# Optimization experiments

Measured on AMD Instinct MI355X. Metric: run time of the kernel, lower is better.

The kernel has to match this reference:

```python
import jax, jax.numpy as jnp
import numpy as np
import math

B, H, N, D = 2, 16, 8192, 64
NUM_PROJS = 7
BLOCK = 256   # key block size
SAMPLE = 256  # number of sampled columns


def _gray_perm(n):
    # AngularLSH._unit_hamming_distance_array: Gray-code ordering of 2**n buckets
    a = np.array([0, 1], dtype=np.int32)
    for i in range(1, n):
        a = np.concatenate([a, a[::-1] + 2 ** i])
    return a

PERM = jnp.asarray(_gray_perm(NUM_PROJS))
ENC = jnp.asarray(2 ** np.arange(NUM_PROJS), dtype=jnp.int32)


def lsh_hash(x, proj_dir):
    # sign-bit angular LSH, then Gray-code remap so nearby buckets share bits
    bits = (jnp.einsum('bhnd,dr->bhnr', x, proj_dir) > 0).astype(jnp.int32)
    bin_ids = (bits * ENC).sum(-1)
    return PERM[bin_ids]


def take_seq(x, idx):
    # gather along the sequence axis (axis=2); idx is [B,H,M]
    return jnp.take_along_axis(x, idx[..., None], axis=2)


def setup_inputs() -> dict:
    key = jax.random.key(0)
    ks = jax.random.split(key, 5)
    return {
        'query': jax.random.normal(ks[0], (B, H, N, D), jnp.float32),
        'key': jax.random.normal(ks[1], (B, H, N, D), jnp.float32),
        'value': jax.random.normal(ks[2], (B, H, N, D), jnp.float32),
        'proj_dir': jax.random.normal(ks[3], (D + 1, NUM_PROJS), jnp.float32),
        'sampled_set': jax.random.randint(ks[4], (B, H, SAMPLE), 0, N),
    }


def reference(query, key, value, proj_dir, sampled_set):
    scale = D ** -0.5

    # asymmetric MIPS transform: key gets sqrt(max||k||^2 - ||k||^2), query gets 0
    k_norm = jnp.linalg.norm(key, axis=-1)                 # [B,H,N]
    k_max = jnp.max(k_norm, axis=-1, keepdims=True)        # [B,H,1]
    k_extra = jnp.sqrt(jnp.maximum(k_max ** 2 - k_norm ** 2, 0.0))
    key_aug = jnp.concatenate([key, k_extra[..., None]], axis=-1)
    query_aug = jnp.concatenate([query, jnp.zeros_like(query[..., :1])], axis=-1)

    # stable sort by LSH bucket; inverse permutation to un-sort queries at the end
    q_idx = jnp.argsort(lsh_hash(query_aug, proj_dir), axis=2, stable=True)
    k_idx = jnp.argsort(lsh_hash(key_aug, proj_dir), axis=2, stable=True)
    q_idx_inv = jnp.argsort(q_idx, axis=2, stable=True)

    q_s = take_seq(query, q_idx)
    k_s = take_seq(key, k_idx)
    v_s = take_seq(value, k_idx)

    nb = N // BLOCK      # number of key blocks (N divisible by BLOCK here)
    qbs = N // nb        # query block size

    # 1) block-diagonal exact attention over LSH-sorted blocks
    qb = q_s.reshape(B, H, nb, qbs, D)
    kb = k_s.reshape(B, H, nb, BLOCK, D)
    vb = v_s.reshape(B, H, nb, BLOCK, D)
    s_blk = jnp.einsum('bhgqd,bhgkd->bhgqk', qb, kb) * scale
    lse_blk = jax.nn.logsumexp(s_blk, axis=-1)             # [B,H,nb,qbs]
    attn_blk = jnp.einsum('bhgqk,bhgkd->bhgqd', jax.nn.softmax(s_blk, axis=-1), vb)
    attn_blk = attn_blk.reshape(B, H, N, D)
    lse_blk = lse_blk.reshape(B, H, N, 1)

    # 2) residual via uniformly sampled columns; mask out columns already in the
    #    query's own diagonal block to avoid double counting
    k_sub = take_seq(k_s, sampled_set)                     # [B,H,S,D]
    v_sub = take_seq(v_s, sampled_set)
    q_blk_id = jnp.arange(N) // qbs                        # [N]
    covered = q_blk_id[None, None, :, None] == (sampled_set // BLOCK)[:, :, None, :]
    bias = jnp.where(covered, jnp.finfo(q_s.dtype).min, 0.0)
    s_res = jnp.einsum('bhnd,bhsd->bhns', q_s, k_sub) * scale + bias
    # importance weight n_key/sample_size applied in log-space (approximate_unsampled)
    lse_res = jax.nn.logsumexp(s_res, axis=-1, keepdims=True) + math.log(N / SAMPLE)
    attn_res = jnp.einsum('bhns,bhsd->bhnd', jax.nn.softmax(s_res, axis=-1), v_sub)

    # add_self_attentions: merge the two softmax estimates in log-space
    c = 1.0 / (1.0 + jnp.exp(lse_res - lse_blk))
    attn = c * attn_blk + (1.0 - c) * attn_res

    # un-sort rows back to the original query order
    attn = take_seq(attn, q_idx_inv)
    return attn
```

## Files before the change

kernel.cpp:

```cpp
#include <hip/hip_runtime.h>
#include <hip/hip_bf16.h>
#include <math.h>

#define BD 2
#define HD 16
#define NSEQ 8192
#define DDIM 64
#define NPROJ 7
#define KBLK 256
#define NSAMP 256
#define NBH (BD*HD)
#define NB (NSEQ/KBLK)

typedef short bf16x8 __attribute__((ext_vector_type(8)));
typedef float f32x4 __attribute__((ext_vector_type(4)));

__device__ __forceinline__ unsigned int pk2bf(float a, float b) {
    union { __hip_bfloat162 h; unsigned int u; } t;
    t.h = __float22bfloat162_rn(make_float2(a, b));
    return t.u;
}

__global__ __launch_bounds__(256) void prelude_kernel(const float* __restrict__ q,
                                                      const float* __restrict__ k,
                                                      const float* __restrict__ pd,
                                                      float* __restrict__ kdots,
                                                      unsigned int* __restrict__ kmax_bits,
                                                      unsigned char* __restrict__ qh) {
    __shared__ float pds[(DDIM+1)*NPROJ];
    __shared__ float red[256];
    const int tid = threadIdx.x;
    for (int i = tid; i < (DDIM+1)*NPROJ; i += 256) pds[i] = pd[i];
    __syncthreads();

    const int lin = blockIdx.x * 256 + tid;
    const int bh = lin >> 13;

    float acc[NPROJ];
    float4 xv[16];

    {
        const float4* xp = (const float4*)(q + (size_t)lin * DDIM);
        #pragma unroll
        for (int j = 0; j < 16; ++j) xv[j] = xp[j];
        #pragma unroll
        for (int r = 0; r < NPROJ; ++r) acc[r] = 0.f;
        #pragma unroll
        for (int j = 0; j < 16; ++j) {
            float xs[4] = {xv[j].x, xv[j].y, xv[j].z, xv[j].w};
            #pragma unroll
            for (int c = 0; c < 4; ++c) {
                const int d = j*4 + c;
                #pragma unroll
                for (int r = 0; r < NPROJ; ++r) acc[r] += xs[c] * pds[d*NPROJ + r];
            }
        }
        int bin = 0;
        #pragma unroll
        for (int r = 0; r < NPROJ; ++r) bin |= (acc[r] > 0.f) << r;
        qh[lin] = (unsigned char)(bin ^ (bin >> 1));
    }

    float nr;
    {
        const float4* xp = (const float4*)(k + (size_t)lin * DDIM);
        #pragma unroll
        for (int j = 0; j < 16; ++j) xv[j] = xp[j];
        #pragma unroll
        for (int r = 0; r < NPROJ; ++r) acc[r] = 0.f;
        #pragma unroll
        for (int j = 0; j < 16; ++j) {
            float xs[4] = {xv[j].x, xv[j].y, xv[j].z, xv[j].w};
            #pragma unroll
            for (int c = 0; c < 4; ++c) {
                const int d = j*4 + c;
                #pragma unroll
                for (int r = 0; r < NPROJ; ++r) acc[r] += xs[c] * pds[d*NPROJ + r];
            }
        }
        float ss = 0.f;
        #pragma unroll
        for (int j = 0; j < 16; ++j) {
            float4 t = xv[j];
            ss += t.x*t.x + t.y*t.y + t.z*t.z + t.w*t.w;
        }
        nr = sqrtf(ss);
        float4* kd = (float4*)(kdots + (size_t)lin * 8);
        kd[0] = make_float4(acc[0], acc[1], acc[2], acc[3]);
        kd[1] = make_float4(acc[4], acc[5], acc[6], nr);
    }

    red[tid] = nr;
    __syncthreads();
    for (int s = 128; s > 0; s >>= 1) {
        if (tid < s) red[tid] = fmaxf(red[tid], red[tid+s]);
        __syncthreads();
    }
    if (tid == 0) atomicMax(&kmax_bits[bh], __float_as_uint(red[0]));
}

__global__ __launch_bounds__(256) void khash_kernel(const float* __restrict__ pd,
                                                    const float* __restrict__ kdots,
                                                    const unsigned int* __restrict__ kmax_bits,
                                                    unsigned char* __restrict__ kh) {
    const int lin = blockIdx.x * 256 + threadIdx.x;
    const int bh = lin >> 13;
    const float4* kd = (const float4*)(kdots + (size_t)lin * 8);
    float4 d0 = kd[0], d1 = kd[1];
    float acc[NPROJ] = {d0.x, d0.y, d0.z, d0.w, d1.x, d1.y, d1.z};
    const float kn = d1.w;
    const float km = __uint_as_float(kmax_bits[bh]);
    const float ex = sqrtf(fmaxf(km*km - kn*kn, 0.f));
    int bin = 0;
    #pragma unroll
    for (int r = 0; r < NPROJ; ++r) {
        acc[r] += ex * pd[DDIM*NPROJ + r];
        bin |= (acc[r] > 0.f) << r;
    }
    kh[lin] = (unsigned char)(bin ^ (bin >> 1));
}

__global__ __launch_bounds__(256) void sort_kernel(const unsigned char* __restrict__ qhash,
                                                   const unsigned char* __restrict__ khash,
                                                   int* __restrict__ qidx,
                                                   int* __restrict__ kidx) {
    __shared__ unsigned char hsh[NSEQ];
    __shared__ unsigned short cnt[128][264];
    __shared__ int base[128];
    __shared__ int wtot[2];
    const int bh = blockIdx.x, tid = threadIdx.x;
    const unsigned char* hash = blockIdx.y ? khash : qhash;
    int* idx = blockIdx.y ? kidx : qidx;

    {
        const uint4* src = (const uint4*)(hash + (size_t)bh * NSEQ);
        uint4* hdst = (uint4*)hsh;
        hdst[tid] = src[tid];
        hdst[tid + 256] = src[tid + 256];
        unsigned int* cz = (unsigned int*)&cnt[0][0];
        for (int i = tid; i < 128*264/2; i += 256) cz[i] = 0;
    }
    __syncthreads();
    {
        const unsigned char* s = hsh + tid*32;
        for (int i = 0; i < 32; ++i) cnt[s[i]][tid]++;
    }
    __syncthreads();

    int sc = 0, vv = 0;
    if (tid < 128) {
        unsigned run = 0;
        uint4* rp = (uint4*)cnt[tid];
        for (int wd = 0; wd < 32; ++wd) {
            uint4 x = rp[wd];
            unsigned v0 = x.x & 0xffffu, v1 = x.x >> 16;
            unsigned v2 = x.y & 0xffffu, v3 = x.y >> 16;
            unsigned v4 = x.z & 0xffffu, v5 = x.z >> 16;
            unsigned v6 = x.w & 0xffffu, v7 = x.w >> 16;
            unsigned p0 = run, p1 = p0+v0, p2 = p1+v1, p3 = p2+v2,
                     p4 = p3+v3, p5 = p4+v4, p6 = p5+v5, p7 = p6+v6;
            run = p7 + v7;
            x.x = p0 | (p1<<16); x.y = p2 | (p3<<16);
            x.z = p4 | (p5<<16); x.w = p6 | (p7<<16);
            rp[wd] = x;
        }
        vv = (int)run;
        sc = vv;
        #pragma unroll
        for (int d = 1; d < 64; d <<= 1) {
            int t = __shfl_up(sc, d, 64);
            if ((tid & 63) >= d) sc += t;
        }
        if ((tid & 63) == 63) wtot[tid >> 6] = sc;
    }
    __syncthreads();
    if (tid < 128) base[tid] = (sc - vv) + (tid >= 64 ? wtot[0] : 0);
    __syncthreads();
    {
        int* dst = idx + (size_t)bh * NSEQ;
        const unsigned char* s = hsh + tid*32;
        for (int i = 0; i < 32; ++i) {
            int h = s[i];
            int c = cnt[h][tid];
            cnt[h][tid] = (unsigned short)(c + 1);
            dst[base[h] + c] = tid*32 + i;
        }
    }
}

#define VSWZ(d) ((((d) >> 1) & 7) << 4)

__global__ __launch_bounds__(256) void respack_kernel(const float* __restrict__ k,
                                                      const float* __restrict__ v,
                                                      const int* __restrict__ samp,
                                                      const int* __restrict__ kidx,
                                                      char* __restrict__ kres,
                                                      char* __restrict__ vres) {
    const int bh = blockIdx.x, ch = blockIdx.y, tid = threadIdx.x;
    const size_t basef = (size_t)bh * NSEQ * DDIM;
    char* kimg = kres + (size_t)(bh*4 + ch) * 8192;
    char* vimg = vres + (size_t)(bh*4 + ch) * 8192;

    {
        const int kk = tid & 63, dc = tid >> 6;
        const int sp = samp[bh*NSAMP + ch*64 + kk];
        const int row = kidx[bh*NSEQ + sp];
        const float* kr = k + basef + (size_t)row*DDIM + dc*16;
        float4 f0 = ((const float4*)kr)[0], f1 = ((const float4*)kr)[1];
        float4 f2 = ((const float4*)kr)[2], f3 = ((const float4*)kr)[3];
        union { bf16x8 v8; unsigned int u[4]; } h0, h1;
        h0.u[0] = pk2bf(f0.x,f0.y); h0.u[1] = pk2bf(f0.z,f0.w);
        h0.u[2] = pk2bf(f1.x,f1.y); h0.u[3] = pk2bf(f1.z,f1.w);
        h1.u[0] = pk2bf(f2.x,f2.y); h1.u[1] = pk2bf(f2.z,f2.w);
        h1.u[2] = pk2bf(f3.x,f3.y); h1.u[3] = pk2bf(f3.z,f3.w);
        const int rb = kk*128 + dc*32, sw = (kk & 7) << 4;
        *(bf16x8*)(kimg + ((rb) ^ sw)) = h0.v8;
        *(bf16x8*)(kimg + ((rb + 16) ^ sw)) = h1.v8;
    }
    {
        const int vg = tid & 15, kq = tid >> 4;
        const int r0 = kidx[bh*NSEQ + samp[bh*NSAMP + ch*64 + kq*4 + 0]];
        const int r1 = kidx[bh*NSEQ + samp[bh*NSAMP + ch*64 + kq*4 + 1]];
        const int r2 = kidx[bh*NSEQ + samp[bh*NSAMP + ch*64 + kq*4 + 2]];
        const int r3 = kidx[bh*NSEQ + samp[bh*NSAMP + ch*64 + kq*4 + 3]];
        float4 x0 = *(const float4*)(v + basef + (size_t)r0*DDIM + vg*4);
        float4 x1 = *(const float4*)(v + basef + (size_t)r1*DDIM + vg*4);
        float4 x2 = *(const float4*)(v + basef + (size_t)r2*DDIM + vg*4);
        float4 x3 = *(const float4*)(v + basef + (size_t)r3*DDIM + vg*4);
        const float c0[4] = {x0.x, x0.y, x0.z, x0.w};
        const float c1[4] = {x1.x, x1.y, x1.z, x1.w};
        const float c2[4] = {x2.x, x2.y, x2.z, x2.w};
        const float c3[4] = {x3.x, x3.y, x3.z, x3.w};
        #pragma unroll
        for (int j = 0; j < 4; ++j) {
            const int d = vg*4 + j;
            unsigned h01 = pk2bf(c0[j], c1[j]);
            unsigned h23 = pk2bf(c2[j], c3[j]);
            *(uint2*)(vimg + ((d*128 + kq*8) ^ VSWZ(d))) = make_uint2(h01, h23);
        }
    }
}


#define PPITCH 80
#define LN32 3.46573590279972f

template<int PHASE>
__device__ __forceinline__ void chunk_compute(
    int lane, char* Pw, int ch,
    const bf16x8 (&qhf)[4][2], const bf16x8 (&qlf)[4][2],
    f32x4 (&O)[4][4], float (&lacc)[4],
    const float* maskF, const char* KhL, const char* VthL) {

    const int lr4 = lane >> 4;
    const int lc  = lane & 15;

    #pragma unroll
    for (int half = 0; half < 2; ++half) {
        #pragma unroll
        for (int m2 = 0; m2 < 2; ++m2) {
            const int mt = half*2 + m2;
            const int key = mt*16 + lc;
            const int ksw = (key & 7) << 4;
            bf16x8 ka0 = *(const bf16x8*)(KhL + ((key*128 +  0 + lr4*16) ^ ksw));
            bf16x8 ka1 = *(const bf16x8*)(KhL + ((key*128 + 64 + lr4*16) ^ ksw));
            float4 mk;
            if (PHASE) mk = *(const float4*)(maskF + ch*64 + mt*16 + lr4*4);
            #pragma unroll
            for (int qt = 0; qt < 4; ++qt) {
                f32x4 c = {0.f, 0.f, 0.f, 0.f};
                c = __builtin_amdgcn_mfma_f32_16x16x32_bf16(ka0, qhf[qt][0], c, 0, 0, 0);
                c = __builtin_amdgcn_mfma_f32_16x16x32_bf16(ka0, qlf[qt][0], c, 0, 0, 0);
                c = __builtin_amdgcn_mfma_f32_16x16x32_bf16(ka1, qhf[qt][1], c, 0, 0, 0);
                c = __builtin_amdgcn_mfma_f32_16x16x32_bf16(ka1, qlf[qt][1], c, 0, 0, 0);
                float e0, e1, e2, e3;
                if (PHASE) {
                    e0 = __expf(c[0] + LN32) * mk.x;
                    e1 = __expf(c[1] + LN32) * mk.y;
                    e2 = __expf(c[2] + LN32) * mk.z;
                    e3 = __expf(c[3] + LN32) * mk.w;
                } else {
                    e0 = __expf(c[0]); e1 = __expf(c[1]);
                    e2 = __expf(c[2]); e3 = __expf(c[3]);
                }
                lacc[qt] += (e0+e1) + (e2+e3);
                uint2 wv;
                wv.x = pk2bf(e0, e1);
                wv.y = pk2bf(e2, e3);
                const int qq = qt*16 + lc;
                *(uint2*)(Pw + qq*PPITCH + m2*32 + lr4*8) = wv;
            }
        }

        bf16x8 pf[4];
        #pragma unroll
        for (int qt = 0; qt < 4; ++qt)
            pf[qt] = *(const bf16x8*)(Pw + (qt*16 + lc)*PPITCH + lr4*16);

        __builtin_amdgcn_s_setprio(1);
        #pragma unroll
        for (int dt = 0; dt < 4; ++dt) {
            const int d = dt*16 + lc;
            const int a = (d*128 + half*64 + lr4*16) ^ VSWZ(d);
            bf16x8 vh = *(const bf16x8*)(VthL + a);
            #pragma unroll
            for (int qt = 0; qt < 4; ++qt) {
                O[qt][dt] = __builtin_amdgcn_mfma_f32_16x16x32_bf16(pf[qt], vh, O[qt][dt], 0, 0, 0);
            }
        }
        __builtin_amdgcn_s_setprio(0);
    }
}

__global__ __launch_bounds__(256, 2) void attn_kernel(const float* __restrict__ q,
                                                      const float* __restrict__ k,
                                                      const float* __restrict__ v,
                                                      const int* __restrict__ samp,
                                                      const int* __restrict__ qidx,
                                                      const int* __restrict__ kidx,
                                                      const char* __restrict__ kres,
                                                      const char* __restrict__ vres,
                                                      float* __restrict__ out) {
    __shared__ __align__(16) char KhL[8192];
    __shared__ __align__(16) char VthL[8192];
    __shared__ __align__(16) char PL[4][PPITCH*64];
    __shared__ int qidxL[256];
    __shared__ int kidxL[256];
    __shared__ float maskF[256];

    const int g = blockIdx.x, bh = blockIdx.y;
    const int tid = threadIdx.x;
    const int lane = tid & 63, w = tid >> 6;
    const int lr4 = lane >> 4, lc = lane & 15;
    const size_t basef = (size_t)bh * NSEQ * DDIM;

    qidxL[tid] = qidx[bh*NSEQ + g*KBLK + tid];
    kidxL[tid] = kidx[bh*NSEQ + g*KBLK + tid];
    {
        int sp = samp[bh*NSAMP + tid];
        maskF[tid] = ((sp >> 8) == g) ? 0.f : 1.f;
    }
    __syncthreads();

    bf16x8 qhf[4][2], qlf[4][2];
    #pragma unroll
    for (int qt = 0; qt < 4; ++qt) {
        const int qrow = qidxL[w*64 + qt*16 + lc];
        const float* qp = q + basef + (size_t)qrow*DDIM;
        #pragma unroll
        for (int ks = 0; ks < 2; ++ks) {
            const float* p = qp + ks*32 + lr4*8;
            float4 a = *(const float4*)p;
            float4 b = *(const float4*)(p + 4);
            float xs[8] = {a.x,a.y,a.z,a.w,b.x,b.y,b.z,b.w};
            union { bf16x8 v8; unsigned int u[4]; } hv, lv;
            #pragma unroll
            for (int j = 0; j < 4; ++j) {
                float s0 = xs[2*j]   * 0.125f;
                float s1 = xs[2*j+1] * 0.125f;
                unsigned hp = pk2bf(s0, s1);
                hv.u[j] = hp;
                float l0 = s0 - __uint_as_float(hp << 16);
                float l1 = s1 - __uint_as_float(hp & 0xffff0000u);
                lv.u[j] = pk2bf(l0, l1);
            }
            qhf[qt][ks] = hv.v8; qlf[qt][ks] = lv.v8;
        }
    }

    f32x4 O[4][4];
    #pragma unroll
    for (int a = 0; a < 4; ++a)
        #pragma unroll
        for (int b = 0; b < 4; ++b) O[a][b] = (f32x4){0.f,0.f,0.f,0.f};
    float lacc[4] = {0,0,0,0};
    char* Pw = PL[w];

    for (int ch = 0; ch < 4; ++ch) {
        __syncthreads();
        {
            const int kk = tid & 63, dc = tid >> 6;
            const int korig = kidxL[ch*64 + kk];
            const float* kr = k + basef + (size_t)korig*DDIM + dc*16;
            float4 f0 = ((const float4*)kr)[0], f1 = ((const float4*)kr)[1];
            float4 f2 = ((const float4*)kr)[2], f3 = ((const float4*)kr)[3];
            union { bf16x8 v8; unsigned int u[4]; } h0, h1;
            h0.u[0] = pk2bf(f0.x,f0.y); h0.u[1] = pk2bf(f0.z,f0.w);
            h0.u[2] = pk2bf(f1.x,f1.y); h0.u[3] = pk2bf(f1.z,f1.w);
            h1.u[0] = pk2bf(f2.x,f2.y); h1.u[1] = pk2bf(f2.z,f2.w);
            h1.u[2] = pk2bf(f3.x,f3.y); h1.u[3] = pk2bf(f3.z,f3.w);
            const int rb = kk*128 + dc*32, sw = (kk & 7) << 4;
            *(bf16x8*)(KhL + ((rb) ^ sw)) = h0.v8;
            *(bf16x8*)(KhL + ((rb + 16) ^ sw)) = h1.v8;
        }
        {
            const int vg = tid & 15, kq = tid >> 4;
            const int r0 = kidxL[ch*64 + kq*4 + 0];
            const int r1 = kidxL[ch*64 + kq*4 + 1];
            const int r2 = kidxL[ch*64 + kq*4 + 2];
            const int r3 = kidxL[ch*64 + kq*4 + 3];
            float4 x0 = *(const float4*)(v + basef + (size_t)r0*DDIM + vg*4);
            float4 x1 = *(const float4*)(v + basef + (size_t)r1*DDIM + vg*4);
            float4 x2 = *(const float4*)(v + basef + (size_t)r2*DDIM + vg*4);
            float4 x3 = *(const float4*)(v + basef + (size_t)r3*DDIM + vg*4);
            const float c0[4] = {x0.x, x0.y, x0.z, x0.w};
            const float c1[4] = {x1.x, x1.y, x1.z, x1.w};
            const float c2[4] = {x2.x, x2.y, x2.z, x2.w};
            const float c3[4] = {x3.x, x3.y, x3.z, x3.w};
            #pragma unroll
            for (int j = 0; j < 4; ++j) {
                const int d = vg*4 + j;
                unsigned h01 = pk2bf(c0[j], c1[j]);
                unsigned h23 = pk2bf(c2[j], c3[j]);
                *(uint2*)(VthL + ((d*128 + kq*8) ^ VSWZ(d))) = make_uint2(h01, h23);
            }
        }
        __syncthreads();
        chunk_compute<0>(lane, Pw, ch, qhf, qlf, O, lacc, maskF, KhL, VthL);
    }

    for (int ch = 0; ch < 4; ++ch) {
        __syncthreads();
        {
            const char* ks = kres + (size_t)(bh*4 + ch) * 8192 + tid*32;
            const char* vs = vres + (size_t)(bh*4 + ch) * 8192 + tid*32;
            float4 a0 = *(const float4*)ks;
            float4 a1 = *(const float4*)(ks + 16);
            float4 b0 = *(const float4*)vs;
            float4 b1 = *(const float4*)(vs + 16);
            *(float4*)(KhL + tid*32)       = a0;
            *(float4*)(KhL + tid*32 + 16)  = a1;
            *(float4*)(VthL + tid*32)      = b0;
            *(float4*)(VthL + tid*32 + 16) = b1;
        }
        __syncthreads();
        chunk_compute<1>(lane, Pw, ch, qhf, qlf, O, lacc, maskF, KhL, VthL);
    }

    #pragma unroll
    for (int qt = 0; qt < 4; ++qt) {
        lacc[qt] += __shfl_xor(lacc[qt], 16, 64);
        lacc[qt] += __shfl_xor(lacc[qt], 32, 64);
        lacc[qt] = 1.f / lacc[qt];
    }
    float* ob = out + basef;
    #pragma unroll
    for (int qt = 0; qt < 4; ++qt) {
        #pragma unroll
        for (int r = 0; r < 4; ++r) {
            const float f = __shfl(lacc[qt], (lane & 48) | (lr4*4 + r), 64);
            const int orow = qidxL[w*64 + qt*16 + lr4*4 + r];
            float* p = ob + (size_t)orow*DDIM + lc;
            #pragma unroll
            for (int dt = 0; dt < 4; ++dt) p[dt*16] = O[qt][dt][r] * f;
        }
    }
}

extern "C" void kernel_launch(void* const* d_in, const int* in_sizes, int n_in,
                              void* d_out, int out_size, void* d_ws, size_t ws_size,
                              hipStream_t stream) {
    const float* q    = (const float*)d_in[0];
    const float* k    = (const float*)d_in[1];
    const float* v    = (const float*)d_in[2];
    const float* pd   = (const float*)d_in[3];
    const int*   samp = (const int*)d_in[4];
    float* out = (float*)d_out;

    char* ws = (char*)d_ws;
    float*         kdots = (float*)(ws + 0);
    int*           qidx  = (int*)(ws + 0);
    int*           kidx  = (int*)(ws + 1048576);
    char*          kres  = ws + 2097152;
    char*          vres  = ws + 3145728;
    unsigned char* qh    = (unsigned char*)(ws + 8388608);
    unsigned char* kh    = (unsigned char*)(ws + 8650752);
    unsigned int*  kmaxb = (unsigned int*)(ws + 8912896);

    hipMemsetAsync(kmaxb, 0, NBH*sizeof(unsigned int), stream);
    hipLaunchKernelGGL(prelude_kernel, dim3(NBH*NSEQ/256), dim3(256), 0, stream,
                       q, k, pd, kdots, kmaxb, qh);
    hipLaunchKernelGGL(khash_kernel, dim3(NBH*NSEQ/256), dim3(256), 0, stream,
                       pd, kdots, kmaxb, kh);
    hipLaunchKernelGGL(sort_kernel, dim3(NBH, 2), dim3(256), 0, stream, qh, kh, qidx, kidx);
    hipLaunchKernelGGL(respack_kernel, dim3(NBH, 4), dim3(256), 0, stream,
                       k, v, samp, kidx, kres, vres);
    hipLaunchKernelGGL(attn_kernel, dim3(NB, NBH), dim3(256), 0, stream,
                       q, k, v, samp, qidx, kidx, kres, vres, out);
}
```

Baseline: 152.3 us.

## Double-buffer K/V tiles and keep P in registers via transposed 16x16x16 MFMA

Key and value staging moves to two shared-memory buffers. The next chunk's global loads are issued before the current chunk's compute and written to LDS afterwards, which overlaps gather latency with MFMA work and removes one barrier per chunk. The P matrix no longer round-trips through a per-wave LDS scratch buffer. The PV product is computed transposed with 16x16x16 bf16 MFMAs, so the exp results feed the matrix unit straight from registers. The output becomes float4 row stores without shuffles. The cost is more registers for the in-flight loads and twice as many PV MFMA instructions, each half as wide.

```diff
diff --git a/kernel.cpp b/kernel.cpp
--- a/kernel.cpp
+++ b/kernel.cpp
@@ -13,6 +13,7 @@
 #define NB (NSEQ/KBLK)
 
 typedef short bf16x8 __attribute__((ext_vector_type(8)));
+typedef short bf16x4 __attribute__((ext_vector_type(4)));
 typedef float f32x4 __attribute__((ext_vector_type(4)));
 
 __device__ __forceinline__ unsigned int pk2bf(float a, float b) {
@@ -242,12 +243,11 @@
 }
 
 
-#define PPITCH 80
 #define LN32 3.46573590279972f
 
 template<int PHASE>
-__device__ __forceinline__ void chunk_compute(
-    int lane, char* Pw, int ch,
+__device__ __forceinline__ void compute_chunk(
+    int ch, int lane,
     const bf16x8 (&qhf)[4][2], const bf16x8 (&qlf)[4][2],
     f32x4 (&O)[4][4], float (&lacc)[4],
     const float* maskF, const char* KhL, const char* VthL) {
@@ -256,57 +256,47 @@
     const int lc  = lane & 15;
 
     #pragma unroll
-    for (int half = 0; half < 2; ++half) {
-        #pragma unroll
-        for (int m2 = 0; m2 < 2; ++m2) {
-            const int mt = half*2 + m2;
-            const int key = mt*16 + lc;
-            const int ksw = (key & 7) << 4;
-            bf16x8 ka0 = *(const bf16x8*)(KhL + ((key*128 +  0 + lr4*16) ^ ksw));
-            bf16x8 ka1 = *(const bf16x8*)(KhL + ((key*128 + 64 + lr4*16) ^ ksw));
-            float4 mk;
-            if (PHASE) mk = *(const float4*)(maskF + ch*64 + mt*16 + lr4*4);
-            #pragma unroll
-            for (int qt = 0; qt < 4; ++qt) {
-                f32x4 c = {0.f, 0.f, 0.f, 0.f};
-                c = __builtin_amdgcn_mfma_f32_16x16x32_bf16(ka0, qhf[qt][0], c, 0, 0, 0);
-                c = __builtin_amdgcn_mfma_f32_16x16x32_bf16(ka0, qlf[qt][0], c, 0, 0, 0);
-                c = __builtin_amdgcn_mfma_f32_16x16x32_bf16(ka1, qhf[qt][1], c, 0, 0, 0);
-                c = __builtin_amdgcn_mfma_f32_16x16x32_bf16(ka1, qlf[qt][1], c, 0, 0, 0);
-                float e0, e1, e2, e3;
-                if (PHASE) {
-                    e0 = __expf(c[0] + LN32) * mk.x;
-                    e1 = __expf(c[1] + LN32) * mk.y;
-                    e2 = __expf(c[2] + LN32) * mk.z;
-                    e3 = __expf(c[3] + LN32) * mk.w;
-                } else {
-                    e0 = __expf(c[0]); e1 = __expf(c[1]);
-                    e2 = __expf(c[2]); e3 = __expf(c[3]);
-                }
-                lacc[qt] += (e0+e1) + (e2+e3);
-                uint2 wv;
-                wv.x = pk2bf(e0, e1);
-                wv.y = pk2bf(e2, e3);
-                const int qq = qt*16 + lc;
-                *(uint2*)(Pw + qq*PPITCH + m2*32 + lr4*8) = wv;
+    for (int mt = 0; mt < 4; ++mt) {
+        const int key = mt*16 + lc;
+        const int ksw = (key & 7) << 4;
+        bf16x8 ka0 = *(const bf16x8*)(KhL + ((key*128 +  0 + lr4*16) ^ ksw));
+        bf16x8 ka1 = *(const bf16x8*)(KhL + ((key*128 + 64 + lr4*16) ^ ksw));
+        float4 mk;
+        if (PHASE) mk = *(const float4*)(maskF + ch*64 + mt*16 + lr4*4);
+
+        bf16x4 pb[4];
+        #pragma unroll
+        for (int qt = 0; qt < 4; ++qt) {
+            f32x4 c = {0.f, 0.f, 0.f, 0.f};
+            c = __builtin_amdgcn_mfma_f32_16x16x32_bf16(ka0, qhf[qt][0], c, 0, 0, 0);
+            c = __builtin_amdgcn_mfma_f32_16x16x32_bf16(ka0, qlf[qt][0], c, 0, 0, 0);
+            c = __builtin_amdgcn_mfma_f32_16x16x32_bf16(ka1, qhf[qt][1], c, 0, 0, 0);
+            c = __builtin_amdgcn_mfma_f32_16x16x32_bf16(ka1, qlf[qt][1], c, 0, 0, 0);
+            float e0, e1, e2, e3;
+            if (PHASE) {
+                e0 = __expf(c[0] + LN32) * mk.x;
+                e1 = __expf(c[1] + LN32) * mk.y;
+                e2 = __expf(c[2] + LN32) * mk.z;
+                e3 = __expf(c[3] + LN32) * mk.w;
+            } else {
+                e0 = __expf(c[0]); e1 = __expf(c[1]);
+                e2 = __expf(c[2]); e3 = __expf(c[3]);
             }
-        }
-
-        bf16x8 pf[4];
-        #pragma unroll
-        for (int qt = 0; qt < 4; ++qt)
-            pf[qt] = *(const bf16x8*)(Pw + (qt*16 + lc)*PPITCH + lr4*16);
+            lacc[qt] += (e0+e1) + (e2+e3);
+            union { bf16x4 v4; unsigned int u[2]; } pw;
+            pw.u[0] = pk2bf(e0, e1);
+            pw.u[1] = pk2bf(e2, e3);
+            pb[qt] = pw.v4;
+        }
 
         __builtin_amdgcn_s_setprio(1);
         #pragma unroll
         for (int dt = 0; dt < 4; ++dt) {
             const int d = dt*16 + lc;
-            const int a = (d*128 + half*64 + lr4*16) ^ VSWZ(d);
-            bf16x8 vh = *(const bf16x8*)(VthL + a);
+            bf16x4 va = *(const bf16x4*)(VthL + ((d*128 + mt*32 + lr4*8) ^ VSWZ(d)));
             #pragma unroll
-            for (int qt = 0; qt < 4; ++qt) {
-                O[qt][dt] = __builtin_amdgcn_mfma_f32_16x16x32_bf16(pf[qt], vh, O[qt][dt], 0, 0, 0);
-            }
+            for (int qt = 0; qt < 4; ++qt)
+                O[qt][dt] = __builtin_amdgcn_mfma_f32_16x16x16bf16_1k(va, pb[qt], O[qt][dt], 0, 0, 0);
         }
         __builtin_amdgcn_s_setprio(0);
     }
@@ -321,9 +311,8 @@
                                                       const char* __restrict__ kres,
                                                       const char* __restrict__ vres,
                                                       float* __restrict__ out) {
-    __shared__ __align__(16) char KhL[8192];
-    __shared__ __align__(16) char VthL[8192];
-    __shared__ __align__(16) char PL[4][PPITCH*64];
+    __shared__ __align__(16) char KB[2][8192];
+    __shared__ __align__(16) char VB[2][8192];
     __shared__ int qidxL[256];
     __shared__ int kidxL[256];
     __shared__ float maskF[256];
@@ -374,68 +363,93 @@
         #pragma unroll
         for (int b = 0; b < 4; ++b) O[a][b] = (f32x4){0.f,0.f,0.f,0.f};
     float lacc[4] = {0,0,0,0};
-    char* Pw = PL[w];
-
-    for (int ch = 0; ch < 4; ++ch) {
-        __syncthreads();
-        {
-            const int kk = tid & 63, dc = tid >> 6;
-            const int korig = kidxL[ch*64 + kk];
-            const float* kr = k + basef + (size_t)korig*DDIM + dc*16;
-            float4 f0 = ((const float4*)kr)[0], f1 = ((const float4*)kr)[1];
-            float4 f2 = ((const float4*)kr)[2], f3 = ((const float4*)kr)[3];
-            union { bf16x8 v8; unsigned int u[4]; } h0, h1;
-            h0.u[0] = pk2bf(f0.x,f0.y); h0.u[1] = pk2bf(f0.z,f0.w);
-            h0.u[2] = pk2bf(f1.x,f1.y); h0.u[3] = pk2bf(f1.z,f1.w);
-            h1.u[0] = pk2bf(f2.x,f2.y); h1.u[1] = pk2bf(f2.z,f2.w);
-            h1.u[2] = pk2bf(f3.x,f3.y); h1.u[3] = pk2bf(f3.z,f3.w);
-            const int rb = kk*128 + dc*32, sw = (kk & 7) << 4;
-            *(bf16x8*)(KhL + ((rb) ^ sw)) = h0.v8;
-            *(bf16x8*)(KhL + ((rb + 16) ^ sw)) = h1.v8;
-        }
-        {
-            const int vg = tid & 15, kq = tid >> 4;
-            const int r0 = kidxL[ch*64 + kq*4 + 0];
-            const int r1 = kidxL[ch*64 + kq*4 + 1];
-            const int r2 = kidxL[ch*64 + kq*4 + 2];
-            const int r3 = kidxL[ch*64 + kq*4 + 3];
-            float4 x0 = *(const float4*)(v + basef + (size_t)r0*DDIM + vg*4);
-            float4 x1 = *(const float4*)(v + basef + (size_t)r1*DDIM + vg*4);
-            float4 x2 = *(const float4*)(v + basef + (size_t)r2*DDIM + vg*4);
-            float4 x3 = *(const float4*)(v + basef + (size_t)r3*DDIM + vg*4);
-            const float c0[4] = {x0.x, x0.y, x0.z, x0.w};
-            const float c1[4] = {x1.x, x1.y, x1.z, x1.w};
-            const float c2[4] = {x2.x, x2.y, x2.z, x2.w};
-            const float c3[4] = {x3.x, x3.y, x3.z, x3.w};
-            #pragma unroll
-            for (int j = 0; j < 4; ++j) {
-                const int d = vg*4 + j;
-                unsigned h01 = pk2bf(c0[j], c1[j]);
-                unsigned h23 = pk2bf(c2[j], c3[j]);
-                *(uint2*)(VthL + ((d*128 + kq*8) ^ VSWZ(d))) = make_uint2(h01, h23);
-            }
-        }
-        __syncthreads();
-        chunk_compute<0>(lane, Pw, ch, qhf, qlf, O, lacc, maskF, KhL, VthL);
-    }
-
-    for (int ch = 0; ch < 4; ++ch) {
-        __syncthreads();
-        {
-            const char* ks = kres + (size_t)(bh*4 + ch) * 8192 + tid*32;
-            const char* vs = vres + (size_t)(bh*4 + ch) * 8192 + tid*32;
-            float4 a0 = *(const float4*)ks;
-            float4 a1 = *(const float4*)(ks + 16);
-            float4 b0 = *(const float4*)vs;
-            float4 b1 = *(const float4*)(vs + 16);
-            *(float4*)(KhL + tid*32)       = a0;
-            *(float4*)(KhL + tid*32 + 16)  = a1;
-            *(float4*)(VthL + tid*32)      = b0;
-            *(float4*)(VthL + tid*32 + 16) = b1;
-        }
-        __syncthreads();
-        chunk_compute<1>(lane, Pw, ch, qhf, qlf, O, lacc, maskF, KhL, VthL);
-    }
+
+    const int kk = tid & 63, dcw = tid >> 6;
+    const int vg = tid & 15, kq = tid >> 4;
+
+    #define BD_LOAD(CH, KF0,KF1,KF2,KF3, VX0,VX1,VX2,VX3)                         \
+        {                                                                          \
+            const int korig = kidxL[(CH)*64 + kk];                                 \
+            const float* kr = k + basef + (size_t)korig*DDIM + dcw*16;             \
+            KF0 = ((const float4*)kr)[0]; KF1 = ((const float4*)kr)[1];            \
+            KF2 = ((const float4*)kr)[2]; KF3 = ((const float4*)kr)[3];            \
+            VX0 = *(const float4*)(v + basef + (size_t)kidxL[(CH)*64+kq*4+0]*DDIM + vg*4); \
+            VX1 = *(const float4*)(v + basef + (size_t)kidxL[(CH)*64+kq*4+1]*DDIM + vg*4); \
+            VX2 = *(const float4*)(v + basef + (size_t)kidxL[(CH)*64+kq*4+2]*DDIM + vg*4); \
+            VX3 = *(const float4*)(v + basef + (size_t)kidxL[(CH)*64+kq*4+3]*DDIM + vg*4); \
+        }
+
+    #define BD_WRITE(BUF, KF0,KF1,KF2,KF3, VX0,VX1,VX2,VX3)                       \
+        {                                                                          \
+            union { bf16x8 v8; unsigned int u[4]; } h0, h1;                        \
+            h0.u[0] = pk2bf(KF0.x,KF0.y); h0.u[1] = pk2bf(KF0.z,KF0.w);            \
+            h0.u[2] = pk2bf(KF1.x,KF1.y); h0.u[3] = pk2bf(KF1.z,KF1.w);            \
+            h1.u[0] = pk2bf(KF2.x,KF2.y); h1.u[1] = pk2bf(KF2.z,KF2.w);            \
+            h1.u[2] = pk2bf(KF3.x,KF3.y); h1.u[3] = pk2bf(KF3.z,KF3.w);            \
+            const int rb = kk*128 + dcw*32, sw2 = (kk & 7) << 4;                   \
+            *(bf16x8*)(KB[BUF] + ((rb) ^ sw2)) = h0.v8;                            \
+            *(bf16x8*)(KB[BUF] + ((rb + 16) ^ sw2)) = h1.v8;                       \
+            const float c0[4] = {VX0.x, VX0.y, VX0.z, VX0.w};                      \
+            const float c1[4] = {VX1.x, VX1.y, VX1.z, VX1.w};                      \
+            const float c2[4] = {VX2.x, VX2.y, VX2.z, VX2.w};                      \
+            const float c3[4] = {VX3.x, VX3.y, VX3.z, VX3.w};                      \
+            _Pragma("unroll")                                                      \
+            for (int j = 0; j < 4; ++j) {                                          \
+                const int d = vg*4 + j;                                            \
+                unsigned h01 = pk2bf(c0[j], c1[j]);                                \
+                unsigned h23 = pk2bf(c2[j], c3[j]);                                \
+                *(uint2*)(VB[BUF] + ((d*128 + kq*8) ^ VSWZ(d))) = make_uint2(h01, h23); \
+            }                                                                      \
+        }
+
+    #define RES_LOAD(RCH, KF0,KF1, VX0,VX1)                                       \
+        {                                                                          \
+            const char* ksrc = kres + (size_t)(bh*4 + (RCH)) * 8192 + tid*32;      \
+            const char* vsrc = vres + (size_t)(bh*4 + (RCH)) * 8192 + tid*32;      \
+            KF0 = ((const float4*)ksrc)[0]; KF1 = ((const float4*)ksrc)[1];        \
+            VX0 = ((const float4*)vsrc)[0]; VX1 = ((const float4*)vsrc)[1];        \
+        }
+
+    #define RES_WRITE(BUF, KF0,KF1, VX0,VX1)                                      \
+        {                                                                          \
+            *(float4*)(KB[BUF] + tid*32)      = KF0;                               \
+            *(float4*)(KB[BUF] + tid*32 + 16) = KF1;                               \
+            *(float4*)(VB[BUF] + tid*32)      = VX0;                               \
+            *(float4*)(VB[BUF] + tid*32 + 16) = VX1;                               \
+        }
+
+    {
+        float4 a0,a1,a2,a3, b0,b1,b2,b3;
+        BD_LOAD(0, a0,a1,a2,a3, b0,b1,b2,b3)
+        BD_WRITE(0, a0,a1,a2,a3, b0,b1,b2,b3)
+    }
+    __syncthreads();
+
+    #define STEP(C)                                                               \
+    {                                                                             \
+        float4 a0,a1,a2,a3, b0,b1,b2,b3;                                          \
+        if ((C) < 7) {                                                            \
+            if ((C) + 1 < 4) { BD_LOAD((C)+1, a0,a1,a2,a3, b0,b1,b2,b3) }         \
+            else             { RES_LOAD((C)+1-4, a0,a1, b0,b1) }                  \
+        }                                                                         \
+        if ((C) < 4) compute_chunk<0>((C),   lane, qhf, qlf, O, lacc, maskF,      \
+                                      KB[(C)&1], VB[(C)&1]);                      \
+        else         compute_chunk<1>((C)-4, lane, qhf, qlf, O, lacc, maskF,      \
+                                      KB[(C)&1], VB[(C)&1]);                      \
+        if ((C) < 7) {                                                            \
+            if ((C) + 1 < 4) { BD_WRITE(((C)+1)&1, a0,a1,a2,a3, b0,b1,b2,b3) }    \
+            else             { RES_WRITE(((C)+1)&1, a0,a1, b0,b1) }               \
+            __syncthreads();                                                      \
+        }                                                                         \
+    }
+
+    STEP(0) STEP(1) STEP(2) STEP(3) STEP(4) STEP(5) STEP(6) STEP(7)
+
+    #undef STEP
+    #undef BD_LOAD
+    #undef BD_WRITE
+    #undef RES_LOAD
+    #undef RES_WRITE
 
     #pragma unroll
     for (int qt = 0; qt < 4; ++qt) {
@@ -446,13 +460,14 @@
     float* ob = out + basef;
     #pragma unroll
     for (int qt = 0; qt < 4; ++qt) {
-        #pragma unroll
-        for (int r = 0; r < 4; ++r) {
-            const float f = __shfl(lacc[qt], (lane & 48) | (lr4*4 + r), 64);
-            const int orow = qidxL[w*64 + qt*16 + lr4*4 + r];
-            float* p = ob + (size_t)orow*DDIM + lc;
-            #pragma unroll
-            for (int dt = 0; dt < 4; ++dt) p[dt*16] = O[qt][dt][r] * f;
+        const int orow = qidxL[w*64 + qt*16 + lc];
+        const float f = lacc[qt];
+        float* p = ob + (size_t)orow*DDIM + lr4*4;
+        #pragma unroll
+        for (int dt = 0; dt < 4; ++dt) {
+            float4 st = make_float4(O[qt][dt][0]*f, O[qt][dt][1]*f,
+                                    O[qt][dt][2]*f, O[qt][dt][3]*f);
+            *(float4*)(p + dt*16) = st;
         }
     }
 }
```

New measurement: 165.8 us. 1.09x slower.

## Keep softmax probabilities in registers and feed PV MFMA directly, dropping LDS P buffer

Applied to the files above, without the earlier changes.

The QK MFMA output layout is reused directly as the B operand of a 16x16x16 bf16 MFMA for the PV product. This removes the per-wave LDS round trip that wrote and reread the probability tile, along with its shared memory. The output is now transposed (O^T), so each lane holds four consecutive d values of one query row. The epilogue therefore drops the per-row lacc shuffles and writes float4 stores. In exchange it uses twice as many smaller K=16 MFMAs and narrower V reads from LDS.

```diff
diff --git a/kernel.cpp b/kernel.cpp
--- a/kernel.cpp
+++ b/kernel.cpp
@@ -13,6 +13,7 @@
 #define NB (NSEQ/KBLK)
 
 typedef short bf16x8 __attribute__((ext_vector_type(8)));
+typedef short bf16x4 __attribute__((ext_vector_type(4)));
 typedef float f32x4 __attribute__((ext_vector_type(4)));
 
 __device__ __forceinline__ unsigned int pk2bf(float a, float b) {
@@ -242,12 +243,11 @@
 }
 
 
-#define PPITCH 80
 #define LN32 3.46573590279972f
 
 template<int PHASE>
-__device__ __forceinline__ void chunk_compute(
-    int lane, char* Pw, int ch,
+__device__ __forceinline__ void compute_chunk(
+    int ch, int lane,
     const bf16x8 (&qhf)[4][2], const bf16x8 (&qlf)[4][2],
     f32x4 (&O)[4][4], float (&lacc)[4],
     const float* maskF, const char* KhL, const char* VthL) {
@@ -256,57 +256,47 @@
     const int lc  = lane & 15;
 
     #pragma unroll
-    for (int half = 0; half < 2; ++half) {
-        #pragma unroll
-        for (int m2 = 0; m2 < 2; ++m2) {
-            const int mt = half*2 + m2;
-            const int key = mt*16 + lc;
-            const int ksw = (key & 7) << 4;
-            bf16x8 ka0 = *(const bf16x8*)(KhL + ((key*128 +  0 + lr4*16) ^ ksw));
-            bf16x8 ka1 = *(const bf16x8*)(KhL + ((key*128 + 64 + lr4*16) ^ ksw));
-            float4 mk;
-            if (PHASE) mk = *(const float4*)(maskF + ch*64 + mt*16 + lr4*4);
-            #pragma unroll
-            for (int qt = 0; qt < 4; ++qt) {
-                f32x4 c = {0.f, 0.f, 0.f, 0.f};
-                c = __builtin_amdgcn_mfma_f32_16x16x32_bf16(ka0, qhf[qt][0], c, 0, 0, 0);
-                c = __builtin_amdgcn_mfma_f32_16x16x32_bf16(ka0, qlf[qt][0], c, 0, 0, 0);
-                c = __builtin_amdgcn_mfma_f32_16x16x32_bf16(ka1, qhf[qt][1], c, 0, 0, 0);
-                c = __builtin_amdgcn_mfma_f32_16x16x32_bf16(ka1, qlf[qt][1], c, 0, 0, 0);
-                float e0, e1, e2, e3;
-                if (PHASE) {
-                    e0 = __expf(c[0] + LN32) * mk.x;
-                    e1 = __expf(c[1] + LN32) * mk.y;
-                    e2 = __expf(c[2] + LN32) * mk.z;
-                    e3 = __expf(c[3] + LN32) * mk.w;
-                } else {
-                    e0 = __expf(c[0]); e1 = __expf(c[1]);
-                    e2 = __expf(c[2]); e3 = __expf(c[3]);
-                }
-                lacc[qt] += (e0+e1) + (e2+e3);
-                uint2 wv;
-                wv.x = pk2bf(e0, e1);
-                wv.y = pk2bf(e2, e3);
-                const int qq = qt*16 + lc;
-                *(uint2*)(Pw + qq*PPITCH + m2*32 + lr4*8) = wv;
+    for (int mt = 0; mt < 4; ++mt) {
+        const int key = mt*16 + lc;
+        const int ksw = (key & 7) << 4;
+        bf16x8 ka0 = *(const bf16x8*)(KhL + ((key*128 +  0 + lr4*16) ^ ksw));
+        bf16x8 ka1 = *(const bf16x8*)(KhL + ((key*128 + 64 + lr4*16) ^ ksw));
+        float4 mk;
+        if (PHASE) mk = *(const float4*)(maskF + ch*64 + mt*16 + lr4*4);
+
+        bf16x4 pb[4];
+        #pragma unroll
+        for (int qt = 0; qt < 4; ++qt) {
+            f32x4 c = {0.f, 0.f, 0.f, 0.f};
+            c = __builtin_amdgcn_mfma_f32_16x16x32_bf16(ka0, qhf[qt][0], c, 0, 0, 0);
+            c = __builtin_amdgcn_mfma_f32_16x16x32_bf16(ka0, qlf[qt][0], c, 0, 0, 0);
+            c = __builtin_amdgcn_mfma_f32_16x16x32_bf16(ka1, qhf[qt][1], c, 0, 0, 0);
+            c = __builtin_amdgcn_mfma_f32_16x16x32_bf16(ka1, qlf[qt][1], c, 0, 0, 0);
+            float e0, e1, e2, e3;
+            if (PHASE) {
+                e0 = __expf(c[0] + LN32) * mk.x;
+                e1 = __expf(c[1] + LN32) * mk.y;
+                e2 = __expf(c[2] + LN32) * mk.z;
+                e3 = __expf(c[3] + LN32) * mk.w;
+            } else {
+                e0 = __expf(c[0]); e1 = __expf(c[1]);
+                e2 = __expf(c[2]); e3 = __expf(c[3]);
             }
-        }
-
-        bf16x8 pf[4];
-        #pragma unroll
-        for (int qt = 0; qt < 4; ++qt)
-            pf[qt] = *(const bf16x8*)(Pw + (qt*16 + lc)*PPITCH + lr4*16);
+            lacc[qt] += (e0+e1) + (e2+e3);
+            union { bf16x4 v4; unsigned int u[2]; } pw;
+            pw.u[0] = pk2bf(e0, e1);
+            pw.u[1] = pk2bf(e2, e3);
+            pb[qt] = pw.v4;
+        }
 
         __builtin_amdgcn_s_setprio(1);
         #pragma unroll
         for (int dt = 0; dt < 4; ++dt) {
             const int d = dt*16 + lc;
-            const int a = (d*128 + half*64 + lr4*16) ^ VSWZ(d);
-            bf16x8 vh = *(const bf16x8*)(VthL + a);
+            bf16x4 va = *(const bf16x4*)(VthL + ((d*128 + mt*32 + lr4*8) ^ VSWZ(d)));
             #pragma unroll
-            for (int qt = 0; qt < 4; ++qt) {
-                O[qt][dt] = __builtin_amdgcn_mfma_f32_16x16x32_bf16(pf[qt], vh, O[qt][dt], 0, 0, 0);
-            }
+            for (int qt = 0; qt < 4; ++qt)
+                O[qt][dt] = __builtin_amdgcn_mfma_f32_16x16x16bf16_1k(va, pb[qt], O[qt][dt], 0, 0, 0);
         }
         __builtin_amdgcn_s_setprio(0);
     }
@@ -321,9 +311,8 @@
                                                       const char* __restrict__ kres,
                                                       const char* __restrict__ vres,
                                                       float* __restrict__ out) {
-    __shared__ __align__(16) char KhL[8192];
-    __shared__ __align__(16) char VthL[8192];
-    __shared__ __align__(16) char PL[4][PPITCH*64];
+    __shared__ __align__(16) char KB[8192];
+    __shared__ __align__(16) char VB[8192];
     __shared__ int qidxL[256];
     __shared__ int kidxL[256];
     __shared__ float maskF[256];
@@ -374,14 +363,15 @@
         #pragma unroll
         for (int b = 0; b < 4; ++b) O[a][b] = (f32x4){0.f,0.f,0.f,0.f};
     float lacc[4] = {0,0,0,0};
-    char* Pw = PL[w];
+
+    const int kk = tid & 63, dcw = tid >> 6;
+    const int vg = tid & 15, kq = tid >> 4;
 
     for (int ch = 0; ch < 4; ++ch) {
         __syncthreads();
         {
-            const int kk = tid & 63, dc = tid >> 6;
             const int korig = kidxL[ch*64 + kk];
-            const float* kr = k + basef + (size_t)korig*DDIM + dc*16;
+            const float* kr = k + basef + (size_t)korig*DDIM + dcw*16;
             float4 f0 = ((const float4*)kr)[0], f1 = ((const float4*)kr)[1];
             float4 f2 = ((const float4*)kr)[2], f3 = ((const float4*)kr)[3];
             union { bf16x8 v8; unsigned int u[4]; } h0, h1;
@@ -389,12 +379,11 @@
             h0.u[2] = pk2bf(f1.x,f1.y); h0.u[3] = pk2bf(f1.z,f1.w);
             h1.u[0] = pk2bf(f2.x,f2.y); h1.u[1] = pk2bf(f2.z,f2.w);
             h1.u[2] = pk2bf(f3.x,f3.y); h1.u[3] = pk2bf(f3.z,f3.w);
-            const int rb = kk*128 + dc*32, sw = (kk & 7) << 4;
-            *(bf16x8*)(KhL + ((rb) ^ sw)) = h0.v8;
-            *(bf16x8*)(KhL + ((rb + 16) ^ sw)) = h1.v8;
+            const int rb = kk*128 + dcw*32, sw2 = (kk & 7) << 4;
+            *(bf16x8*)(KB + ((rb) ^ sw2)) = h0.v8;
+            *(bf16x8*)(KB + ((rb + 16) ^ sw2)) = h1.v8;
         }
         {
-            const int vg = tid & 15, kq = tid >> 4;
             const int r0 = kidxL[ch*64 + kq*4 + 0];
             const int r1 = kidxL[ch*64 + kq*4 + 1];
             const int r2 = kidxL[ch*64 + kq*4 + 2];
@@ -412,29 +401,29 @@
                 const int d = vg*4 + j;
                 unsigned h01 = pk2bf(c0[j], c1[j]);
                 unsigned h23 = pk2bf(c2[j], c3[j]);
-                *(uint2*)(VthL + ((d*128 + kq*8) ^ VSWZ(d))) = make_uint2(h01, h23);
+                *(uint2*)(VB + ((d*128 + kq*8) ^ VSWZ(d))) = make_uint2(h01, h23);
             }
         }
         __syncthreads();
-        chunk_compute<0>(lane, Pw, ch, qhf, qlf, O, lacc, maskF, KhL, VthL);
+        compute_chunk<0>(ch, lane, qhf, qlf, O, lacc, maskF, KB, VB);
     }
 
     for (int ch = 0; ch < 4; ++ch) {
         __syncthreads();
         {
-            const char* ks = kres + (size_t)(bh*4 + ch) * 8192 + tid*32;
-            const char* vs = vres + (size_t)(bh*4 + ch) * 8192 + tid*32;
-            float4 a0 = *(const float4*)ks;
-            float4 a1 = *(const float4*)(ks + 16);
-            float4 b0 = *(const float4*)vs;
-            float4 b1 = *(const float4*)(vs + 16);
-            *(float4*)(KhL + tid*32)       = a0;
-            *(float4*)(KhL + tid*32 + 16)  = a1;
-            *(float4*)(VthL + tid*32)      = b0;
-            *(float4*)(VthL + tid*32 + 16) = b1;
+            const char* ksrc = kres + (size_t)(bh*4 + ch) * 8192 + tid*32;
+            const char* vsrc = vres + (size_t)(bh*4 + ch) * 8192 + tid*32;
+            float4 a0 = ((const float4*)ksrc)[0];
+            float4 a1 = ((const float4*)ksrc)[1];
+            float4 b0 = ((const float4*)vsrc)[0];
+            float4 b1 = ((const float4*)vsrc)[1];
+            *(float4*)(KB + tid*32)      = a0;
+            *(float4*)(KB + tid*32 + 16) = a1;
+            *(float4*)(VB + tid*32)      = b0;
+            *(float4*)(VB + tid*32 + 16) = b1;
         }
         __syncthreads();
-        chunk_compute<1>(lane, Pw, ch, qhf, qlf, O, lacc, maskF, KhL, VthL);
+        compute_chunk<1>(ch, lane, qhf, qlf, O, lacc, maskF, KB, VB);
     }
 
     #pragma unroll
@@ -446,13 +435,14 @@
     float* ob = out + basef;
     #pragma unroll
     for (int qt = 0; qt < 4; ++qt) {
-        #pragma unroll
-        for (int r = 0; r < 4; ++r) {
-            const float f = __shfl(lacc[qt], (lane & 48) | (lr4*4 + r), 64);
-            const int orow = qidxL[w*64 + qt*16 + lr4*4 + r];
-            float* p = ob + (size_t)orow*DDIM + lc;
-            #pragma unroll
-            for (int dt = 0; dt < 4; ++dt) p[dt*16] = O[qt][dt][r] * f;
+        const int orow = qidxL[w*64 + qt*16 + lc];
+        const float f = lacc[qt];
+        float* p = ob + (size_t)orow*DDIM + lr4*4;
+        #pragma unroll
+        for (int dt = 0; dt < 4; ++dt) {
+            float4 st = make_float4(O[qt][dt][0]*f, O[qt][dt][1]*f,
+                                    O[qt][dt][2]*f, O[qt][dt][3]*f);
+            *(float4*)(p + dt*16) = st;
         }
     }
 }
```

Measured after the change: 157.5 us. 3.4% more time.
